# Kernel tuning notes

Hardware: AMD Instinct MI355X
Metric: run time of the kernel (lower is better)

Reference implementation:

```python
import jax, jax.numpy as jnp
import numpy as np

NUM_EXPERTS = 8
TOP_K = 2
HIDDEN = 2048
INTER = 1408
TOKENS = 4096


def setup_inputs() -> dict:
    key = jax.random.key(0)
    ks = jax.random.split(key, 5)
    scale_h = 1.0 / np.sqrt(HIDDEN)
    scale_i = 1.0 / np.sqrt(INTER)
    return {
        "x": jax.random.normal(ks[0], (TOKENS, HIDDEN), dtype=jnp.float32),
        "router_w": jax.random.normal(ks[1], (NUM_EXPERTS, HIDDEN), dtype=jnp.float32) * scale_h,
        "w_gate": jax.random.normal(ks[2], (NUM_EXPERTS, HIDDEN, INTER), dtype=jnp.float32) * scale_h,
        "w_up": jax.random.normal(ks[3], (NUM_EXPERTS, HIDDEN, INTER), dtype=jnp.float32) * scale_h,
        "w_down": jax.random.normal(ks[4], (NUM_EXPERTS, INTER, HIDDEN), dtype=jnp.float32) * scale_i,
    }


def reference(x, router_w, w_gate, w_up, w_down):
    # Router: softmax over experts, top-k, renormalize top-k probs
    logits = x @ router_w.T                       # [T, E]
    probs = jax.nn.softmax(logits, axis=-1)
    top_vals, top_idx = jax.lax.top_k(probs, TOP_K)  # [T, K]
    top_vals = top_vals / jnp.sum(top_vals, axis=-1, keepdims=True)
    # Combine weights: [T, E], zero for unselected experts
    t_ar = jnp.arange(x.shape[0])[:, None]
    combine = jnp.zeros((x.shape[0], NUM_EXPERTS), dtype=x.dtype).at[t_ar, top_idx].add(top_vals)
    # Expert SwiGLU FFN: down( silu(x@gate) * (x@up) ), weighted combine.
    # Loop over the small fixed expert set (8); each iteration is a dense GEMM chain.
    out = jnp.zeros_like(x)
    for e in range(NUM_EXPERTS):
        h = jax.nn.silu(x @ w_gate[e]) * (x @ w_up[e])  # [T, INTER]
        out = out + combine[:, e:e + 1] * (h @ w_down[e])
    return out
```

## Files before the change

kernel.cpp:

```cpp
#include <hip/hip_runtime.h>
#include <hip/hip_bf16.h>
#include <cstdint>
#include <cstddef>

#define TOKENS 4096
#define HIDDEN 2048
#define INTER  1408
#define NE     8
#define NGU    2816
#define CAP_ROWS 9216

typedef __bf16 bf16;
typedef __bf16 bf16x8 __attribute__((ext_vector_type(8)));
typedef float  f32x4  __attribute__((ext_vector_type(4)));

__device__ __forceinline__ void async16(const void* g, void* l) {
  __builtin_amdgcn_global_load_lds((const __attribute__((address_space(1))) void*)g,
                                   (__attribute__((address_space(3))) void*)l,
                                   16, 0, 0);
}

__global__ void router_kernel(const float* __restrict__ x, const float* __restrict__ rw,
                              bf16* __restrict__ xb, int* __restrict__ cnt,
                              int* __restrict__ tok, float* __restrict__ wts) {
  const int w = threadIdx.x >> 6, l = threadIdx.x & 63;
  const int t = blockIdx.x * 4 + w;
  const float4* x4 = (const float4*)(x + (size_t)t * HIDDEN);
  const float4* r4 = (const float4*)rw;
  float acc[NE];
#pragma unroll
  for (int e = 0; e < NE; ++e) acc[e] = 0.f;
#pragma unroll
  for (int c = 0; c < 8; ++c) {
    const int idx = c * 64 + l;
    const float4 v = x4[idx];
    bf16* dst = xb + (size_t)t * HIDDEN + idx * 4;
    dst[0] = (bf16)v.x; dst[1] = (bf16)v.y; dst[2] = (bf16)v.z; dst[3] = (bf16)v.w;
#pragma unroll
    for (int e = 0; e < NE; ++e) {
      const float4 u = r4[e * 512 + idx];
      acc[e] += v.x * u.x + v.y * u.y + v.z * u.z + v.w * u.w;
    }
  }
#pragma unroll
  for (int e = 0; e < NE; ++e)
#pragma unroll
    for (int s = 32; s > 0; s >>= 1) acc[e] += __shfl_xor(acc[e], s, 64);
  if (l == 0) {
    int i0 = 0; float l0 = acc[0];
#pragma unroll
    for (int e = 1; e < NE; ++e) if (acc[e] > l0) { l0 = acc[e]; i0 = e; }
    int i1 = -1; float l1 = -3.4e38f;
#pragma unroll
    for (int e = 0; e < NE; ++e) if (e != i0 && acc[e] > l1) { l1 = acc[e]; i1 = e; }
    const float w0 = 1.f / (1.f + __expf(l1 - l0));
    const float w1 = 1.f - w0;
    int p = atomicAdd(&cnt[i0], 1); tok[i0 * 4096 + p] = t; wts[i0 * 4096 + p] = w0;
    p = atomicAdd(&cnt[i1], 1);     tok[i1 * 4096 + p] = t; wts[i1 * 4096 + p] = w1;
  }
}

__global__ void scan_kernel(const int* __restrict__ cnt, int* __restrict__ offs) {
  if (threadIdx.x == 0 && blockIdx.x == 0) {
    int o = 0;
    for (int e = 0; e < NE; ++e) { offs[e] = o; o += ((cnt[e] + 127) >> 7) << 7; }
    offs[NE] = o;
  }
}

__global__ void transpose_cvt(const float* __restrict__ in, bf16* __restrict__ out,
                              int R, int C, size_t inStride, size_t outStride) {
  __shared__ float tile[32][33];
  const float* src = in + blockIdx.z * inStride;
  bf16* dst = out + blockIdx.z * outStride;
  const int c0 = blockIdx.x * 32, r0 = blockIdx.y * 32;
#pragma unroll
  for (int yy = 0; yy < 32; yy += 8)
    tile[threadIdx.y + yy][threadIdx.x] =
        src[(size_t)(r0 + threadIdx.y + yy) * C + c0 + threadIdx.x];
  __syncthreads();
#pragma unroll
  for (int yy = 0; yy < 32; yy += 8)
    dst[(size_t)(c0 + threadIdx.y + yy) * R + r0 + threadIdx.x] =
        (bf16)tile[threadIdx.x][threadIdx.y + yy];
}

__global__ __launch_bounds__(256, 2) void gemm_gateup(
    const bf16* __restrict__ X, const bf16* __restrict__ W, bf16* __restrict__ H,
    const int* __restrict__ cnt, const int* __restrict__ offs, const int* __restrict__ tok) {
  const int e = blockIdx.z, mt = blockIdx.y, nt = blockIdx.x;
  const int c = cnt[e];
  if (mt * 128 >= c) return;

  __shared__ bf16 sA[128 * 32];
  __shared__ bf16 sB[128 * 32];

  const int t = threadIdx.x, l = t & 63, w = t >> 6;
  const int iA0 = t, iA1 = t + 256;
  const int rA0 = iA0 >> 2, g0 = iA0 & 3;
  const int rA1 = iA1 >> 2, g1 = iA1 & 3;
  const int gr0 = tok[e * 4096 + (mt * 128 + rA0 < c ? mt * 128 + rA0 : c - 1)];
  const int gr1 = tok[e * 4096 + (mt * 128 + rA1 < c ? mt * 128 + rA1 : c - 1)];
  const bf16* pa0 = X + (size_t)gr0 * HIDDEN + g0 * 8;
  const bf16* pa1 = X + (size_t)gr1 * HIDDEN + g1 * 8;
  const bf16* pb0 = W + ((size_t)e * NGU + nt * 128 + rA0) * HIDDEN + g0 * 8;
  const bf16* pb1 = W + ((size_t)e * NGU + nt * 128 + rA1) * HIDDEN + g1 * 8;
  bf16* la0 = sA + iA0 * 8; bf16* la1 = sA + iA1 * 8;
  bf16* lb0 = sB + iA0 * 8; bf16* lb1 = sB + iA1 * 8;

  const int wm = (w >> 1) * 64, wn = (w & 1) * 64;
  const int r16 = l & 15, quad = l >> 4;
  const bf16* fA = sA + (wm + r16) * 32 + quad * 8;
  const bf16* fB = sB + (wn + r16) * 32 + quad * 8;

  f32x4 acc[4][4];
#pragma unroll
  for (int i = 0; i < 4; ++i)
#pragma unroll
    for (int j = 0; j < 4; ++j) acc[i][j] = (f32x4){0.f, 0.f, 0.f, 0.f};

  for (int kk = 0; kk < HIDDEN; kk += 32) {
    async16(pa0 + kk, la0); async16(pa1 + kk, la1);
    async16(pb0 + kk, lb0); async16(pb1 + kk, lb1);
    __syncthreads();
    bf16x8 a[4], b[4];
#pragma unroll
    for (int i = 0; i < 4; ++i) a[i] = *(const bf16x8*)(fA + i * 16 * 32);
#pragma unroll
    for (int j = 0; j < 4; ++j) b[j] = *(const bf16x8*)(fB + j * 16 * 32);
#pragma unroll
    for (int i = 0; i < 4; ++i)
#pragma unroll
      for (int j = 0; j < 4; ++j)
        acc[i][j] = __builtin_amdgcn_mfma_f32_16x16x32_bf16(a[i], b[j], acc[i][j], 0, 0, 0);
    __syncthreads();
  }

  const int rowBase = offs[e] + mt * 128 + wm + quad * 4;
  const int colBase = nt * 128 + wn + r16;
#pragma unroll
  for (int i = 0; i < 4; ++i)
#pragma unroll
    for (int r = 0; r < 4; ++r) {
      bf16* dst = H + (size_t)(rowBase + i * 16 + r) * NGU + colBase;
#pragma unroll
      for (int j = 0; j < 4; ++j) dst[j * 16] = (bf16)acc[i][j][r];
    }
}

__global__ void silu_mul(const bf16* __restrict__ Hraw, bf16* __restrict__ H) {
  const int v = blockIdx.x * blockDim.x + threadIdx.x;
  const int r = v / 176;
  const int cc = v - r * 176;
  const bf16x8 g8 = *(const bf16x8*)(Hraw + (size_t)r * NGU + cc * 8);
  const bf16x8 u8 = *(const bf16x8*)(Hraw + (size_t)r * NGU + INTER + cc * 8);
  bf16x8 o;
#pragma unroll
  for (int i = 0; i < 8; ++i) {
    const float g = (float)g8[i];
    const float u = (float)u8[i];
    o[i] = (bf16)((g / (1.f + __expf(-g))) * u);
  }
  *(bf16x8*)(H + (size_t)r * INTER + cc * 8) = o;
}

__global__ __launch_bounds__(256, 2) void gemm_down(
    const bf16* __restrict__ Hin, const bf16* __restrict__ W, float* __restrict__ out,
    const int* __restrict__ cnt, const int* __restrict__ offs,
    const int* __restrict__ tok, const float* __restrict__ wts) {
  const int e = blockIdx.z, mt = blockIdx.y, nt = blockIdx.x;
  const int c = cnt[e];
  if (mt * 128 >= c) return;

  __shared__ bf16 sA[128 * 32];
  __shared__ bf16 sB[128 * 32];

  const int t = threadIdx.x, l = t & 63, w = t >> 6;
  const int iA0 = t, iA1 = t + 256;
  const int rA0 = iA0 >> 2, g0 = iA0 & 3;
  const int rA1 = iA1 >> 2, g1 = iA1 & 3;
  const int base = offs[e] + mt * 128;
  const bf16* pa0 = Hin + (size_t)(base + rA0) * INTER + g0 * 8;
  const bf16* pa1 = Hin + (size_t)(base + rA1) * INTER + g1 * 8;
  const bf16* pb0 = W + ((size_t)e * HIDDEN + nt * 128 + rA0) * INTER + g0 * 8;
  const bf16* pb1 = W + ((size_t)e * HIDDEN + nt * 128 + rA1) * INTER + g1 * 8;
  bf16* la0 = sA + iA0 * 8; bf16* la1 = sA + iA1 * 8;
  bf16* lb0 = sB + iA0 * 8; bf16* lb1 = sB + iA1 * 8;

  const int wm = (w >> 1) * 64, wn = (w & 1) * 64;
  const int r16 = l & 15, quad = l >> 4;
  const bf16* fA = sA + (wm + r16) * 32 + quad * 8;
  const bf16* fB = sB + (wn + r16) * 32 + quad * 8;

  f32x4 acc[4][4];
#pragma unroll
  for (int i = 0; i < 4; ++i)
#pragma unroll
    for (int j = 0; j < 4; ++j) acc[i][j] = (f32x4){0.f, 0.f, 0.f, 0.f};

  for (int kk = 0; kk < INTER; kk += 32) {
    async16(pa0 + kk, la0); async16(pa1 + kk, la1);
    async16(pb0 + kk, lb0); async16(pb1 + kk, lb1);
    __syncthreads();
    bf16x8 a[4], b[4];
#pragma unroll
    for (int i = 0; i < 4; ++i) a[i] = *(const bf16x8*)(fA + i * 16 * 32);
#pragma unroll
    for (int j = 0; j < 4; ++j) b[j] = *(const bf16x8*)(fB + j * 16 * 32);
#pragma unroll
    for (int i = 0; i < 4; ++i)
#pragma unroll
      for (int j = 0; j < 4; ++j)
        acc[i][j] = __builtin_amdgcn_mfma_f32_16x16x32_bf16(a[i], b[j], acc[i][j], 0, 0, 0);
    __syncthreads();
  }

  const int mBase = mt * 128 + wm + quad * 4;
  const int colBase = nt * 128 + wn + r16;
#pragma unroll
  for (int i = 0; i < 4; ++i)
#pragma unroll
    for (int r = 0; r < 4; ++r) {
      const int m = mBase + i * 16 + r;
      if (m < c) {
        const int tkn = tok[e * 4096 + m];
        const float wgt = wts[e * 4096 + m];
        float* dst = out + (size_t)tkn * HIDDEN + colBase;
#pragma unroll
        for (int j = 0; j < 4; ++j) atomicAdd(dst + j * 16, wgt * acc[i][j][r]);
      }
    }
}

extern "C" void kernel_launch(void* const* d_in, const int* in_sizes, int n_in,
                              void* d_out, int out_size, void* d_ws, size_t ws_size,
                              hipStream_t stream) {
  const float* x  = (const float*)d_in[0];
  const float* rw = (const float*)d_in[1];
  const float* wg = (const float*)d_in[2];
  const float* wu = (const float*)d_in[3];
  const float* wd = (const float*)d_in[4];
  float* out = (float*)d_out;

  char* ws = (char*)d_ws;
  size_t o = 0;
  auto alloc = [&](size_t b) { void* p = ws + o; o += (b + 255) & ~(size_t)255; return p; };
  int*   cnt  = (int*)alloc(NE * 4);
  int*   offs = (int*)alloc((NE + 1) * 4);
  int*   tok  = (int*)alloc((size_t)NE * 4096 * 4);
  float* wts  = (float*)alloc((size_t)NE * 4096 * 4);
  bf16*  xb   = (bf16*)alloc((size_t)TOKENS * HIDDEN * 2);
  bf16*  wgu  = (bf16*)alloc((size_t)NE * NGU * HIDDEN * 2);
  bf16*  wdt  = (bf16*)alloc((size_t)NE * HIDDEN * INTER * 2);
  bf16*  hraw = (bf16*)alloc((size_t)CAP_ROWS * NGU * 2);
  bf16*  h    = (bf16*)alloc((size_t)CAP_ROWS * INTER * 2);

  hipMemsetAsync(cnt, 0, NE * 4, stream);
  hipMemsetAsync(d_out, 0, (size_t)TOKENS * HIDDEN * 4, stream);

  router_kernel<<<TOKENS / 4, 256, 0, stream>>>(x, rw, xb, cnt, tok, wts);
  scan_kernel<<<1, 64, 0, stream>>>(cnt, offs);

  dim3 tb(32, 8);
  transpose_cvt<<<dim3(INTER / 32, HIDDEN / 32, NE), tb, 0, stream>>>(
      wg, wgu, HIDDEN, INTER, (size_t)HIDDEN * INTER, (size_t)NGU * HIDDEN);
  transpose_cvt<<<dim3(INTER / 32, HIDDEN / 32, NE), tb, 0, stream>>>(
      wu, wgu + (size_t)INTER * HIDDEN, HIDDEN, INTER, (size_t)HIDDEN * INTER,
      (size_t)NGU * HIDDEN);
  transpose_cvt<<<dim3(HIDDEN / 32, INTER / 32, NE), tb, 0, stream>>>(
      wd, wdt, INTER, HIDDEN, (size_t)INTER * HIDDEN, (size_t)HIDDEN * INTER);

  gemm_gateup<<<dim3(NGU / 128, TOKENS / 128, NE), 256, 0, stream>>>(xb, wgu, hraw, cnt, offs, tok);
  silu_mul<<<(CAP_ROWS * (INTER / 8)) / 256, 256, 0, stream>>>(hraw, h);
  gemm_down<<<dim3(HIDDEN / 128, TOKENS / 128, NE), 256, 0, stream>>>(h, wdt, out, cnt, offs, tok, wts);
}
```

Measured before the change: 728.4 us.

## Fuse SiLU-mul and routing weight into gate/up GEMM epilogue via interleaved weights

```diff
diff --git a/kernel.cpp b/kernel.cpp
--- a/kernel.cpp
+++ b/kernel.cpp
@@ -68,26 +68,42 @@
   }
 }
 
-__global__ void transpose_cvt(const float* __restrict__ in, bf16* __restrict__ out,
-                              int R, int C, size_t inStride, size_t outStride) {
-  __shared__ float tile[32][33];
-  const float* src = in + blockIdx.z * inStride;
-  bf16* dst = out + blockIdx.z * outStride;
-  const int c0 = blockIdx.x * 32, r0 = blockIdx.y * 32;
-#pragma unroll
-  for (int yy = 0; yy < 32; yy += 8)
-    tile[threadIdx.y + yy][threadIdx.x] =
-        src[(size_t)(r0 + threadIdx.y + yy) * C + c0 + threadIdx.x];
+__global__ __launch_bounds__(256) void transpose64(
+    const float* __restrict__ in, bf16* __restrict__ out, int R, int C,
+    size_t inSlab, size_t outSlab, int mode) {
+  __shared__ float tile[64][68];
+  in  += blockIdx.z * inSlab;
+  out += blockIdx.z * outSlab;
+  const int c0 = blockIdx.x * 64, r0 = blockIdx.y * 64;
+  const int t = threadIdx.x;
+  const int row = t >> 4, cq = t & 15;
+  const float* src = in + (size_t)(r0 + row) * C + c0 + cq * 4;
+#pragma unroll
+  for (int p = 0; p < 4; ++p) {
+    const float4 v = *(const float4*)(src + (size_t)(p * 16) * C);
+    *(float4*)&tile[p * 16 + row][cq * 4] = v;
+  }
   __syncthreads();
-#pragma unroll
-  for (int yy = 0; yy < 32; yy += 8)
-    dst[(size_t)(c0 + threadIdx.y + yy) * R + r0 + threadIdx.x] =
-        (bf16)tile[threadIdx.x][threadIdx.y + yy];
-}
-
-__global__ __launch_bounds__(256, 2) void gemm_gateup(
+  const int oc = t >> 2, rq = t & 3;
+  float vals[16];
+#pragma unroll
+  for (int i = 0; i < 16; ++i) vals[i] = tile[rq * 16 + i][oc];
+  const int c = c0 + oc;
+  int p;
+  if (mode == 0) p = c;
+  else p = ((c >> 4) << 5) + (c & 15) + (mode == 2 ? 16 : 0);
+  bf16x8 o0, o1;
+#pragma unroll
+  for (int i = 0; i < 8; ++i) { o0[i] = (bf16)vals[i]; o1[i] = (bf16)vals[8 + i]; }
+  bf16* dst = out + (size_t)p * R + r0 + rq * 16;
+  *(bf16x8*)dst = o0;
+  *(bf16x8*)(dst + 8) = o1;
+}
+
+__global__ __launch_bounds__(256, 4) void gemm_gateup(
     const bf16* __restrict__ X, const bf16* __restrict__ W, bf16* __restrict__ H,
-    const int* __restrict__ cnt, const int* __restrict__ offs, const int* __restrict__ tok) {
+    const int* __restrict__ cnt, const int* __restrict__ offs,
+    const int* __restrict__ tok, const float* __restrict__ wts) {
   const int e = blockIdx.z, mt = blockIdx.y, nt = blockIdx.x;
   const int c = cnt[e];
   if (mt * 128 >= c) return;
@@ -136,38 +152,29 @@
     __syncthreads();
   }
 
-  const int rowBase = offs[e] + mt * 128 + wm + quad * 4;
-  const int colBase = nt * 128 + wn + r16;
+  const int mLoc = mt * 128 + wm + quad * 4;
+  const int hcol = nt * 64 + (wn >> 1) + r16;
 #pragma unroll
   for (int i = 0; i < 4; ++i)
 #pragma unroll
     for (int r = 0; r < 4; ++r) {
-      bf16* dst = H + (size_t)(rowBase + i * 16 + r) * NGU + colBase;
-#pragma unroll
-      for (int j = 0; j < 4; ++j) dst[j * 16] = (bf16)acc[i][j][r];
+      const int m = mLoc + i * 16 + r;
+      const int mc = m < c ? m : c - 1;
+      const float ws = wts[e * 4096 + mc];
+      const float g0v = acc[i][0][r], u0v = acc[i][1][r];
+      const float g1v = acc[i][2][r], u1v = acc[i][3][r];
+      const float h0 = (g0v / (1.f + __expf(-g0v))) * u0v * ws;
+      const float h1 = (g1v / (1.f + __expf(-g1v))) * u1v * ws;
+      bf16* dst = H + (size_t)(offs[e] + m) * INTER + hcol;
+      dst[0]  = (bf16)h0;
+      dst[16] = (bf16)h1;
     }
 }
 
-__global__ void silu_mul(const bf16* __restrict__ Hraw, bf16* __restrict__ H) {
-  const int v = blockIdx.x * blockDim.x + threadIdx.x;
-  const int r = v / 176;
-  const int cc = v - r * 176;
-  const bf16x8 g8 = *(const bf16x8*)(Hraw + (size_t)r * NGU + cc * 8);
-  const bf16x8 u8 = *(const bf16x8*)(Hraw + (size_t)r * NGU + INTER + cc * 8);
-  bf16x8 o;
-#pragma unroll
-  for (int i = 0; i < 8; ++i) {
-    const float g = (float)g8[i];
-    const float u = (float)u8[i];
-    o[i] = (bf16)((g / (1.f + __expf(-g))) * u);
-  }
-  *(bf16x8*)(H + (size_t)r * INTER + cc * 8) = o;
-}
-
-__global__ __launch_bounds__(256, 2) void gemm_down(
+__global__ __launch_bounds__(256, 4) void gemm_down(
     const bf16* __restrict__ Hin, const bf16* __restrict__ W, float* __restrict__ out,
     const int* __restrict__ cnt, const int* __restrict__ offs,
-    const int* __restrict__ tok, const float* __restrict__ wts) {
+    const int* __restrict__ tok) {
   const int e = blockIdx.z, mt = blockIdx.y, nt = blockIdx.x;
   const int c = cnt[e];
   if (mt * 128 >= c) return;
@@ -224,10 +231,9 @@
       const int m = mBase + i * 16 + r;
       if (m < c) {
         const int tkn = tok[e * 4096 + m];
-        const float wgt = wts[e * 4096 + m];
         float* dst = out + (size_t)tkn * HIDDEN + colBase;
 #pragma unroll
-        for (int j = 0; j < 4; ++j) atomicAdd(dst + j * 16, wgt * acc[i][j][r]);
+        for (int j = 0; j < 4; ++j) atomicAdd(dst + j * 16, acc[i][j][r]);
       }
     }
 }
@@ -252,7 +258,6 @@
   bf16*  xb   = (bf16*)alloc((size_t)TOKENS * HIDDEN * 2);
   bf16*  wgu  = (bf16*)alloc((size_t)NE * NGU * HIDDEN * 2);
   bf16*  wdt  = (bf16*)alloc((size_t)NE * HIDDEN * INTER * 2);
-  bf16*  hraw = (bf16*)alloc((size_t)CAP_ROWS * NGU * 2);
   bf16*  h    = (bf16*)alloc((size_t)CAP_ROWS * INTER * 2);
 
   hipMemsetAsync(cnt, 0, NE * 4, stream);
@@ -261,16 +266,15 @@
   router_kernel<<<TOKENS / 4, 256, 0, stream>>>(x, rw, xb, cnt, tok, wts);
   scan_kernel<<<1, 64, 0, stream>>>(cnt, offs);
 
-  dim3 tb(32, 8);
-  transpose_cvt<<<dim3(INTER / 32, HIDDEN / 32, NE), tb, 0, stream>>>(
-      wg, wgu, HIDDEN, INTER, (size_t)HIDDEN * INTER, (size_t)NGU * HIDDEN);
-  transpose_cvt<<<dim3(INTER / 32, HIDDEN / 32, NE), tb, 0, stream>>>(
-      wu, wgu + (size_t)INTER * HIDDEN, HIDDEN, INTER, (size_t)HIDDEN * INTER,
-      (size_t)NGU * HIDDEN);
-  transpose_cvt<<<dim3(HIDDEN / 32, INTER / 32, NE), tb, 0, stream>>>(
-      wd, wdt, INTER, HIDDEN, (size_t)INTER * HIDDEN, (size_t)HIDDEN * INTER);
-
-  gemm_gateup<<<dim3(NGU / 128, TOKENS / 128, NE), 256, 0, stream>>>(xb, wgu, hraw, cnt, offs, tok);
-  silu_mul<<<(CAP_ROWS * (INTER / 8)) / 256, 256, 0, stream>>>(hraw, h);
-  gemm_down<<<dim3(HIDDEN / 128, TOKENS / 128, NE), 256, 0, stream>>>(h, wdt, out, cnt, offs, tok, wts);
-}
+  transpose64<<<dim3(INTER / 64, HIDDEN / 64, NE), 256, 0, stream>>>(
+      wg, wgu, HIDDEN, INTER, (size_t)HIDDEN * INTER, (size_t)NGU * HIDDEN, 1);
+  transpose64<<<dim3(INTER / 64, HIDDEN / 64, NE), 256, 0, stream>>>(
+      wu, wgu, HIDDEN, INTER, (size_t)HIDDEN * INTER, (size_t)NGU * HIDDEN, 2);
+  transpose64<<<dim3(HIDDEN / 64, INTER / 64, NE), 256, 0, stream>>>(
+      wd, wdt, INTER, HIDDEN, (size_t)INTER * HIDDEN, (size_t)HIDDEN * INTER, 0);
+
+  gemm_gateup<<<dim3(NGU / 128, TOKENS / 128, NE), 256, 0, stream>>>(
+      xb, wgu, h, cnt, offs, tok, wts);
+  gemm_down<<<dim3(HIDDEN / 128, TOKENS / 128, NE), 256, 0, stream>>>(
+      h, wdt, out, cnt, offs, tok);
+}
```

Result: faster. 697.8 us (-4.2%).
